# Performance work log

Measured on AMD Instinct MI355X. Metric: run time of the kernel, lower is better.

Reference implementation:

```python
import jax, jax.numpy as jnp
import numpy as np

V, E, L, H = 128, 512, 8, 8
B, T = 4, 1024
EPS = 0.1  # label smoothing


def _ln(x, s, b):
    mu = x.mean(-1, keepdims=True)
    var = ((x - mu) ** 2).mean(-1, keepdims=True)
    return (x - mu) * jax.lax.rsqrt(var + 1e-5) * s + b


def _forward(inputs, targets, emb, qkv_w, qkv_b, aff1_w, aff1_b, aff2_w, aff2_b,
             ffn1_w, ffn1_b, ffn2_w, ffn2_b, ln1_s, ln1_b, ln2_s, ln2_b, head_w, head_b):
    Bx, Tx = inputs.shape
    x = emb[inputs]                                  # [B,T,E]
    dh = E // H
    mask = jnp.tril(jnp.ones((Tx, Tx), dtype=x.dtype))
    scale = np.float32(1.0 / np.sqrt(dh))
    for l in range(L):
        qkv = x @ qkv_w[l].T + qkv_b[l]              # [B,T,3E]
        qkv = qkv.reshape(Bx, Tx, H, 3 * dh).transpose(0, 2, 1, 3)  # [B,H,T,3dh]
        q, k, v = jnp.split(qkv, 3, axis=-1)
        # NOTE: original multiplies scores by boolean tril mask (zeros, not -inf)
        scores = jnp.einsum('bhqd,bhkd->bhqk', q, k) * mask * scale
        att = jax.nn.softmax(scores, axis=-1) @ v    # [B,H,T,dh]
        att = att.transpose(0, 2, 1, 3).reshape(Bx, Tx, E)
        att = jax.nn.relu(att @ aff1_w[l].T + aff1_b[l]) @ aff2_w[l].T + aff2_b[l]
        out1 = _ln(att + x, ln1_s[l], ln1_b[l])
        out2 = jax.nn.relu(out1 @ ffn1_w[l].T + ffn1_b[l]) @ ffn2_w[l].T + ffn2_b[l]
        x = _ln(out1 + out2, ln2_s[l], ln2_b[l])
    logits = x @ head_w.T + head_b                   # [B,T,V]
    logp = jax.nn.log_softmax(logits, axis=-1)
    nll = -jnp.take_along_axis(logp, targets[..., None], axis=-1)[..., 0]
    smooth = -logp.mean(-1)
    loss = jnp.mean((1.0 - EPS) * nll + EPS * smooth)
    return logits, loss


def setup_inputs() -> dict:
    key = jax.random.key(0)
    ks = jax.random.split(key, 16)
    s = lambda k, shape, fan: (jax.random.normal(k, shape, jnp.float32) / np.sqrt(fan)).astype(jnp.float32)
    return {
        'inputs': jax.random.randint(ks[0], (B, T), 0, V, dtype=jnp.int32).astype(jnp.int64),
        'targets': jax.random.randint(ks[1], (B, T), 0, V, dtype=jnp.int32).astype(jnp.int64),
        'emb': s(ks[2], (V, E), 1.0),
        'qkv_w': s(ks[3], (L, 3 * E, E), E),
        'qkv_b': jnp.zeros((L, 3 * E), jnp.float32),
        'aff1_w': s(ks[4], (L, E, E), E),
        'aff1_b': jnp.zeros((L, E), jnp.float32),
        'aff2_w': s(ks[5], (L, E, E), E),
        'aff2_b': jnp.zeros((L, E), jnp.float32),
        'ffn1_w': s(ks[6], (L, E, E), E),
        'ffn1_b': jnp.zeros((L, E), jnp.float32),
        'ffn2_w': s(ks[7], (L, E, E), E),
        'ffn2_b': jnp.zeros((L, E), jnp.float32),
        'ln1_s': jnp.ones((L, E), jnp.float32),
        'ln1_b': jnp.zeros((L, E), jnp.float32),
        'ln2_s': jnp.ones((L, E), jnp.float32),
        'ln2_b': jnp.zeros((L, E), jnp.float32),
        'head_w': s(ks[8], (V, E), E),
        'head_b': jnp.zeros((V,), jnp.float32),
    }


def reference(inputs, targets, emb, qkv_w, qkv_b, aff1_w, aff1_b, aff2_w, aff2_b,
              ffn1_w, ffn1_b, ffn2_w, ffn2_b, ln1_s, ln1_b, ln2_s, ln2_b, head_w, head_b):
    return _forward(inputs, targets, emb, qkv_w, qkv_b, aff1_w, aff1_b, aff2_w, aff2_b,
                    ffn1_w, ffn1_b, ffn2_w, ffn2_b, ln1_s, ln1_b, ln2_s, ln2_b, head_w, head_b)
```

## Files before the change

kernel.cpp:

```cpp
#include <hip/hip_runtime.h>


#define V_  128
#define E_  512
#define L_  8
#define H_  8
#define B_  4
#define T_  1024
#define N_  (B_*T_)
#define DH_ 64
#define E3_ 1536

typedef __attribute__((ext_vector_type(8))) short   bf16x8;
typedef __attribute__((ext_vector_type(4))) float   floatx4;

#define SW(row,k8) (((row) << 6) + ((((k8) ^ ((row) & 7))) << 3))

__device__ __forceinline__ unsigned short f2bf(float f) {
    union { float f; unsigned int i; } v; v.f = f;
    unsigned int x = v.i;
    return (unsigned short)((x + 0x7fffu + ((x >> 16) & 1u)) >> 16);
}
__device__ __forceinline__ float bf2f(unsigned short u) {
    union { unsigned int i; float f; } v; v.i = ((unsigned int)u) << 16; return v.f;
}
__device__ __forceinline__ void gload_lds16(const void* g, void* l) {
    __builtin_amdgcn_global_load_lds(
        (const __attribute__((address_space(1))) unsigned int*)g,
        (__attribute__((address_space(3))) unsigned int*)l, 16, 0, 0);
}

#define CVT_N0 6291456
#define CVT_N1 2097152
#define CVT_TOT (CVT_N0 + 4*CVT_N1 + V_*E_)
__global__ void cvt_all_kernel(const float* __restrict__ s0, const float* __restrict__ s1,
                               const float* __restrict__ s2, const float* __restrict__ s3,
                               const float* __restrict__ s4, const float* __restrict__ s5,
                               unsigned short* __restrict__ dst) {
    long i = (long)(blockIdx.x * blockDim.x + threadIdx.x) * 4;
    if (i >= CVT_TOT) return;
    const float* src; long off;
    if      (i < CVT_N0)               { src = s0; off = i; }
    else if (i < CVT_N0 + CVT_N1)      { src = s1; off = i - CVT_N0; }
    else if (i < CVT_N0 + 2*CVT_N1)    { src = s2; off = i - CVT_N0 - CVT_N1; }
    else if (i < CVT_N0 + 3*CVT_N1)    { src = s3; off = i - CVT_N0 - 2L*CVT_N1; }
    else if (i < CVT_N0 + 4*CVT_N1)    { src = s4; off = i - CVT_N0 - 3L*CVT_N1; }
    else                               { src = s5; off = i - CVT_N0 - 4L*CVT_N1; }
    float4 v = *(const float4*)(src + off);
    ushort4 o; o.x = f2bf(v.x); o.y = f2bf(v.y); o.z = f2bf(v.z); o.w = f2bf(v.w);
    *(ushort4*)(dst + i) = o;
}

__global__ void embed_kernel(const int* __restrict__ tok, const float* __restrict__ emb,
                             float* __restrict__ xf, unsigned short* __restrict__ xb) {
    int idx = blockIdx.x * blockDim.x + threadIdx.x;
    if (idx >= N_ * E_) return;
    int n = idx >> 9;
    int e = idx & (E_ - 1);
    float v = emb[tok[n] * E_ + e];
    xf[idx] = v; xb[idx] = f2bf(v);
}

template<int BM, int RELU, int WF, int WB>
__global__ __launch_bounds__(256) void gemm_mfma(
    const unsigned short* __restrict__ A, const unsigned short* __restrict__ W,
    const float* __restrict__ bias, float* __restrict__ Cf, unsigned short* __restrict__ Cb,
    int M, int Nout, int K)
{
    constexpr int MI = BM / 64;
    __shared__ unsigned short Asm[2][BM * 64];
    __shared__ unsigned short Bsm[2][64 * 64];
    int tid = threadIdx.x;
    int wv = tid >> 6, ln = tid & 63;
    int lquad = ln >> 4, lmod = ln & 15;
    int m0 = blockIdx.y * BM, n0 = blockIdx.x * 64;

    floatx4 acc[MI][4] = {};

    auto stage = [&](int k0, int pb) {
        #pragma unroll
        for (int c = 0; c < BM / 32; ++c) {
            int cc = tid + 256 * c;
            int r = cc >> 3, k8s = (cc & 7) ^ (r & 7);
            gload_lds16(A + (size_t)(m0 + r) * K + k0 + 8 * k8s,
                        &Asm[pb][2048 * c + 512 * wv]);
        }
        #pragma unroll
        for (int c = 0; c < 2; ++c) {
            int cc = tid + 256 * c;
            int r = cc >> 3, k8s = (cc & 7) ^ (r & 7);
            gload_lds16(W + (size_t)(n0 + r) * K + k0 + 8 * k8s,
                        &Bsm[pb][2048 * c + 512 * wv]);
        }
    };

    int nt = K >> 6;
    stage(0, 0);
    __syncthreads();

    for (int t = 0; t < nt; ++t) {
        int pb = t & 1;
        if (t + 1 < nt) stage((t + 1) << 6, pb ^ 1);
        #pragma unroll
        for (int ks = 0; ks < 2; ++ks) {
            bf16x8 af[MI], bfr[4];
            #pragma unroll
            for (int i = 0; i < MI; ++i)
                af[i] = *(const bf16x8*)&Asm[pb][SW((BM/4) * wv + 16 * i + lmod, ks * 4 + lquad)];
            #pragma unroll
            for (int j = 0; j < 4; ++j)
                bfr[j] = *(const bf16x8*)&Bsm[pb][SW(16 * j + lmod, ks * 4 + lquad)];
            #pragma unroll
            for (int i = 0; i < MI; ++i)
                #pragma unroll
                for (int j = 0; j < 4; ++j)
                    acc[i][j] = __builtin_amdgcn_mfma_f32_16x16x32_bf16(af[i], bfr[j], acc[i][j], 0, 0, 0);
        }
        if (t + 1 < nt) __syncthreads();
    }

    #pragma unroll
    for (int i = 0; i < MI; ++i)
        #pragma unroll
        for (int j = 0; j < 4; ++j) {
            int n = n0 + 16 * j + lmod;
            float bj = bias[n];
            #pragma unroll
            for (int v = 0; v < 4; ++v) {
                int m = m0 + (BM/4) * wv + 16 * i + 4 * lquad + v;
                float val = acc[i][j][v] + bj;
                if (RELU) val = fmaxf(val, 0.f);
                if (WF) Cf[(size_t)m * Nout + n] = val;
                if (WB) Cb[(size_t)m * Nout + n] = f2bf(val);
            }
        }
}

__global__ __launch_bounds__(256) void gemm_qkv(
    const unsigned short* __restrict__ A, const unsigned short* __restrict__ W,
    const float* __restrict__ bias, unsigned short* __restrict__ Cb,
    unsigned short* __restrict__ vt_g, float* __restrict__ vtile, int K)
{
    __shared__ unsigned short Asm[2][128 * 64];
    __shared__ unsigned short Bsm[2][64 * 64];
    __shared__ float vred[4][64];
    int tid = threadIdx.x;
    int wv = tid >> 6, ln = tid & 63;
    int lquad = ln >> 4, lmod = ln & 15;
    int m0 = blockIdx.y * 128, n0 = blockIdx.x * 64;

    floatx4 acc[2][4] = {};

    auto stage = [&](int k0, int pb) {
        #pragma unroll
        for (int c = 0; c < 4; ++c) {
            int cc = tid + 256 * c;
            int r = cc >> 3, k8s = (cc & 7) ^ (r & 7);
            gload_lds16(A + (size_t)(m0 + r) * K + k0 + 8 * k8s,
                        &Asm[pb][2048 * c + 512 * wv]);
        }
        #pragma unroll
        for (int c = 0; c < 2; ++c) {
            int cc = tid + 256 * c;
            int r = cc >> 3, k8s = (cc & 7) ^ (r & 7);
            gload_lds16(W + (size_t)(n0 + r) * K + k0 + 8 * k8s,
                        &Bsm[pb][2048 * c + 512 * wv]);
        }
    };

    int nt = K >> 6;
    stage(0, 0);
    __syncthreads();
    for (int t = 0; t < nt; ++t) {
        int pb = t & 1;
        if (t + 1 < nt) stage((t + 1) << 6, pb ^ 1);
        #pragma unroll
        for (int ks = 0; ks < 2; ++ks) {
            bf16x8 af[2], bfr[4];
            #pragma unroll
            for (int i = 0; i < 2; ++i)
                af[i] = *(const bf16x8*)&Asm[pb][SW(32 * wv + 16 * i + lmod, ks * 4 + lquad)];
            #pragma unroll
            for (int j = 0; j < 4; ++j)
                bfr[j] = *(const bf16x8*)&Bsm[pb][SW(16 * j + lmod, ks * 4 + lquad)];
            #pragma unroll
            for (int i = 0; i < 2; ++i)
                #pragma unroll
                for (int j = 0; j < 4; ++j)
                    acc[i][j] = __builtin_amdgcn_mfma_f32_16x16x32_bf16(af[i], bfr[j], acc[i][j], 0, 0, 0);
        }
        if (t + 1 < nt) __syncthreads();
    }

    if ((n0 % 192) != 128) {
        #pragma unroll
        for (int i = 0; i < 2; ++i)
            #pragma unroll
            for (int j = 0; j < 4; ++j) {
                int n = n0 + 16 * j + lmod;
                float bj = bias[n];
                #pragma unroll
                for (int v = 0; v < 4; ++v) {
                    int m = m0 + 32 * wv + 16 * i + 4 * lquad + v;
                    Cb[(size_t)m * E3_ + n] = f2bf(acc[i][j][v] + bj);
                }
            }
    } else {
        int h = n0 / 192;
        int b = m0 >> 10;
        int bh = b * 8 + h;
        int t0 = m0 & 1023;
        int kt0 = t0 >> 6;
        float sj[4] = {0.f, 0.f, 0.f, 0.f};
        #pragma unroll
        for (int j = 0; j < 4; ++j) {
            float bj = bias[n0 + 16 * j + lmod];
            #pragma unroll
            for (int i = 0; i < 2; ++i) {
                union { unsigned short u[4]; uint2 q; } pk;
                #pragma unroll
                for (int v = 0; v < 4; ++v) {
                    unsigned short r = f2bf(acc[i][j][v] + bj);
                    pk.u[v] = r;
                    sj[j] += bf2f(r);
                }
                int t = t0 + 32 * wv + 16 * i + 4 * lquad;
                *(uint2*)&vt_g[((size_t)(bh * 64 + 16 * j + lmod)) * T_ + t] = pk.q;
            }
        }
        #pragma unroll
        for (int j = 0; j < 4; ++j) {
            sj[j] += __shfl_xor(sj[j], 16);
            sj[j] += __shfl_xor(sj[j], 32);
        }
        if (lquad == 0) {
            #pragma unroll
            for (int j = 0; j < 4; ++j) vred[wv][16 * j + lmod] = sj[j];
        }
        __syncthreads();
        if (tid < 128) {
            int half = tid >> 6, d = tid & 63;
            vtile[((size_t)bh * 16 + kt0 + half) * 64 + d] =
                vred[2 * half][d] + vred[2 * half + 1][d];
        }
    }
}

__global__ __launch_bounds__(256) void attn_mfma(const unsigned short* __restrict__ qkv,
                                                 const unsigned short* __restrict__ vt_g,
                                                 const float* __restrict__ vtile,
                                                 unsigned short* __restrict__ outb)
{
    __shared__ unsigned short Qs[64 * 64];
    __shared__ unsigned short Ks[2][64 * 64];
    __shared__ unsigned short Vs[2][64 * 64];
    __shared__ unsigned short Ps[64 * 64];

    int tid = threadIdx.x;
    int wv = tid >> 6, ln = tid & 63;
    int lquad = ln >> 4, lmod = ln & 15;
    int bh = blockIdx.x;
    int y = blockIdx.y;
    int qt = (y < 8) ? y : 23 - y;
    int b = bh >> 3, h = bh & 7;
    int q0 = qt * 64;
    const float scale = 0.125f;
    size_t base = (size_t)b * T_ * E3_ + h * 192;

    auto stageKV = [&](int k0, int pb) {
        #pragma unroll
        for (int c = 0; c < 2; ++c) {
            int cc = tid + 256 * c;
            int r = cc >> 3, k8s = (cc & 7) ^ (r & 7);
            gload_lds16(qkv + base + (size_t)(k0 + r) * E3_ + 64 + 8 * k8s,
                        &Ks[pb][2048 * c + 512 * wv]);
            gload_lds16(vt_g + ((size_t)(bh * 64 + r)) * T_ + k0 + 8 * k8s,
                        &Vs[pb][2048 * c + 512 * wv]);
        }
    };

    #pragma unroll
    for (int c = 0; c < 2; ++c) {
        int cc = tid + 256 * c;
        int r = cc >> 3, k8s = (cc & 7) ^ (r & 7);
        gload_lds16(qkv + base + (size_t)(q0 + r) * E3_ + 8 * k8s, Qs + 2048 * c + 512 * wv);
    }
    stageKV(0, 0);
    __syncthreads();

    float lrow[4] = {0.f, 0.f, 0.f, 0.f};
    floatx4 Oa[4] = {};

    for (int kt = 0; kt <= qt; ++kt) {
        int pb = kt & 1;
        int k0 = kt * 64;
        if (kt < qt) stageKV(k0 + 64, pb ^ 1);

        floatx4 sacc[4] = {};
        #pragma unroll
        for (int ks = 0; ks < 2; ++ks) {
            bf16x8 aq = *(const bf16x8*)&Qs[SW(16 * wv + lmod, ks * 4 + lquad)];
            #pragma unroll
            for (int j = 0; j < 4; ++j) {
                bf16x8 bk = *(const bf16x8*)&Ks[pb][SW(16 * j + lmod, ks * 4 + lquad)];
                sacc[j] = __builtin_amdgcn_mfma_f32_16x16x32_bf16(aq, bk, sacc[j], 0, 0, 0);
            }
        }
        #pragma unroll
        for (int v = 0; v < 4; ++v) {
            int qg = q0 + 16 * wv + 4 * lquad + v;
            int row = 16 * wv + 4 * lquad + v;
            #pragma unroll
            for (int j = 0; j < 4; ++j) {
                int kg = k0 + 16 * j + lmod;
                float p = (kg <= qg) ? __expf(sacc[j][v] * scale) : 1.0f;
                lrow[v] += p;
                int col = 16 * j + lmod;
                Ps[SW(row, col >> 3) + (col & 7)] = f2bf(p);
            }
        }
        asm volatile("s_waitcnt lgkmcnt(0)" ::: "memory");
        __builtin_amdgcn_s_barrier();

        #pragma unroll
        for (int ks = 0; ks < 2; ++ks) {
            bf16x8 ap = *(const bf16x8*)&Ps[SW(16 * wv + lmod, ks * 4 + lquad)];
            #pragma unroll
            for (int f = 0; f < 4; ++f) {
                bf16x8 bv = *(const bf16x8*)&Vs[pb][SW(16 * f + lmod, ks * 4 + lquad)];
                Oa[f] = __builtin_amdgcn_mfma_f32_16x16x32_bf16(ap, bv, Oa[f], 0, 0, 0);
            }
        }
        if (kt < qt) __syncthreads();
    }

    #pragma unroll
    for (int v = 0; v < 4; ++v)
        #pragma unroll
        for (int msk = 1; msk < 16; msk <<= 1) lrow[v] += __shfl_xor(lrow[v], msk);

    if (qt < 15) {
        float Km = (float)((15 - qt) * 64);
        #pragma unroll
        for (int v = 0; v < 4; ++v) lrow[v] += Km;
        #pragma unroll
        for (int f = 0; f < 4; ++f) {
            float sv = 0.f;
            for (int kt = qt + 1; kt < 16; ++kt)
                sv += vtile[((size_t)bh * 16 + kt) * 64 + 16 * f + lmod];
            #pragma unroll
            for (int v = 0; v < 4; ++v) Oa[f][v] += sv;
        }
    }

    #pragma unroll
    for (int f = 0; f < 4; ++f)
        #pragma unroll
        for (int v = 0; v < 4; ++v) {
            int q = q0 + 16 * wv + 4 * lquad + v;
            outb[(size_t)(b * T_ + q) * E_ + h * DH_ + 16 * f + lmod] = f2bf(Oa[f][v] / lrow[v]);
        }
}

__global__ __launch_bounds__(256) void add_ln_kernel(
    const float* __restrict__ a, const float* __restrict__ r,
    const float* __restrict__ s, const float* __restrict__ bpar,
    float* __restrict__ outF, unsigned short* __restrict__ outB)
{
    int tid = threadIdx.x, wv = tid >> 6, ln = tid & 63;
    int n = blockIdx.x * 4 + wv;
    int e = ln * 8;
    size_t base = (size_t)n * E_ + e;
    float4 a0 = *(const float4*)&a[base],     a1 = *(const float4*)&a[base + 4];
    float4 r0 = *(const float4*)&r[base],     r1 = *(const float4*)&r[base + 4];
    float v[8] = {a0.x + r0.x, a0.y + r0.y, a0.z + r0.z, a0.w + r0.w,
                  a1.x + r1.x, a1.y + r1.y, a1.z + r1.z, a1.w + r1.w};

    float sm = 0.f;
    #pragma unroll
    for (int i = 0; i < 8; ++i) sm += v[i];
    #pragma unroll
    for (int msk = 1; msk < 64; msk <<= 1) sm += __shfl_xor(sm, msk);
    float mu = sm * (1.f / 512.f);

    float ss = 0.f;
    #pragma unroll
    for (int i = 0; i < 8; ++i) { v[i] -= mu; ss += v[i] * v[i]; }
    #pragma unroll
    for (int msk = 1; msk < 64; msk <<= 1) ss += __shfl_xor(ss, msk);
    float rstd = rsqrtf(ss * (1.f / 512.f) + 1e-5f);

    float4 sc0 = *(const float4*)&s[e],    sc1 = *(const float4*)&s[e + 4];
    float4 bp0 = *(const float4*)&bpar[e], bp1 = *(const float4*)&bpar[e + 4];
    float o[8];
    o[0] = v[0] * rstd * sc0.x + bp0.x; o[1] = v[1] * rstd * sc0.y + bp0.y;
    o[2] = v[2] * rstd * sc0.z + bp0.z; o[3] = v[3] * rstd * sc0.w + bp0.w;
    o[4] = v[4] * rstd * sc1.x + bp1.x; o[5] = v[5] * rstd * sc1.y + bp1.y;
    o[6] = v[6] * rstd * sc1.z + bp1.z; o[7] = v[7] * rstd * sc1.w + bp1.w;
    *(float4*)&outF[base]     = make_float4(o[0], o[1], o[2], o[3]);
    *(float4*)&outF[base + 4] = make_float4(o[4], o[5], o[6], o[7]);
    union { unsigned short u[8]; uint4 q; } pk;
    #pragma unroll
    for (int i = 0; i < 8; ++i) pk.u[i] = f2bf(o[i]);
    *(uint4*)&outB[base] = pk.q;
}

__global__ __launch_bounds__(128) void loss_row_kernel(
    const float* __restrict__ logits, const int* __restrict__ tgt,
    float* __restrict__ out_logits, float* __restrict__ rowloss)
{
    int n = blockIdx.x, i = threadIdx.x;
    float x = logits[(size_t)n * V_ + i];
    out_logits[(size_t)n * V_ + i] = x;

    __shared__ float redA[2], redB[2];
    __shared__ float xt;
    int lane = i & 63, w = i >> 6;
    if (i == tgt[n]) xt = x;

    float m = x;
    #pragma unroll
    for (int off = 32; off; off >>= 1) m = fmaxf(m, __shfl_down(m, off, 64));
    if (lane == 0) redA[w] = m;
    __syncthreads();
    m = fmaxf(redA[0], redA[1]);
    __syncthreads();

    float ev = __expf(x - m);
    float se = ev, sx = x;
    #pragma unroll
    for (int off = 32; off; off >>= 1) {
        se += __shfl_down(se, off, 64);
        sx += __shfl_down(sx, off, 64);
    }
    if (lane == 0) { redA[w] = se; redB[w] = sx; }
    __syncthreads();
    if (i == 0) {
        float seT = redA[0] + redA[1], sxT = redB[0] + redB[1];
        float lse = m + __logf(seT);
        float nll = lse - xt;
        float smooth = lse - sxT * (1.f / 128.f);
        rowloss[n] = 0.9f * nll + 0.1f * smooth;
    }
}

__global__ __launch_bounds__(256) void loss_reduce_kernel(
    const float* __restrict__ rowloss, float* __restrict__ out)
{
    int tid = threadIdx.x;
    float sm = 0.f;
    for (int idx = tid; idx < N_; idx += 256) sm += rowloss[idx];
    #pragma unroll
    for (int off = 32; off; off >>= 1) sm += __shfl_down(sm, off, 64);
    __shared__ float red[4];
    int lane = tid & 63, w = tid >> 6;
    if (lane == 0) red[w] = sm;
    __syncthreads();
    if (tid == 0) out[0] = (red[0] + red[1] + red[2] + red[3]) * (1.f / (float)N_);
}

extern "C" void kernel_launch(void* const* d_in, const int* in_sizes, int n_in,
                              void* d_out, int out_size, void* d_ws, size_t ws_size,
                              hipStream_t stream)
{
    (void)in_sizes; (void)n_in; (void)out_size; (void)ws_size;
    const int* toks     = (const int*)d_in[0];
    const int* tgts     = (const int*)d_in[1];
    const float* emb    = (const float*)d_in[2];
    const float* qkv_w  = (const float*)d_in[3];
    const float* qkv_b  = (const float*)d_in[4];
    const float* aff1_w = (const float*)d_in[5];
    const float* aff1_b = (const float*)d_in[6];
    const float* aff2_w = (const float*)d_in[7];
    const float* aff2_b = (const float*)d_in[8];
    const float* ffn1_w = (const float*)d_in[9];
    const float* ffn1_b = (const float*)d_in[10];
    const float* ffn2_w = (const float*)d_in[11];
    const float* ffn2_b = (const float*)d_in[12];
    const float* ln1_s  = (const float*)d_in[13];
    const float* ln1_b  = (const float*)d_in[14];
    const float* ln2_s  = (const float*)d_in[15];
    const float* ln2_b  = (const float*)d_in[16];
    const float* head_w = (const float*)d_in[17];
    const float* head_b = (const float*)d_in[18];

    char* p = (char*)d_ws;
    auto carve = [&](size_t bytes) { char* r = p; p += (bytes + 255) & ~(size_t)255; return (void*)r; };
    unsigned short* wb_all  = (unsigned short*)carve((size_t)CVT_TOT * 2);
    unsigned short* wb_qkv  = wb_all;
    unsigned short* wb_aff1 = wb_qkv  + (size_t)CVT_N0;
    unsigned short* wb_aff2 = wb_aff1 + (size_t)CVT_N1;
    unsigned short* wb_ffn1 = wb_aff2 + (size_t)CVT_N1;
    unsigned short* wb_ffn2 = wb_ffn1 + (size_t)CVT_N1;
    unsigned short* wb_head = wb_ffn2 + (size_t)CVT_N1;
    float*          x_f     = (float*)carve((size_t)N_ * E_ * 4);
    unsigned short* x_b     = (unsigned short*)carve((size_t)N_ * E_ * 2);
    unsigned short* qkv_bf  = (unsigned short*)carve((size_t)N_ * E3_ * 2);
    unsigned short* att_b   = (unsigned short*)carve((size_t)N_ * E_ * 2);
    unsigned short* h_b     = (unsigned short*)carve((size_t)N_ * E_ * 2);
    float*          y_f     = (float*)carve((size_t)N_ * E_ * 4);
    float*          o1_f    = (float*)carve((size_t)N_ * E_ * 4);
    unsigned short* o1_b    = (unsigned short*)carve((size_t)N_ * E_ * 2);
    float*          logits  = (float*)carve((size_t)N_ * V_ * 4);
    float*          rowl    = (float*)carve((size_t)N_ * 4);
    float*          vtile   = (float*)carve((size_t)32 * 16 * 64 * 4);
    unsigned short* vt_g    = (unsigned short*)carve((size_t)32 * 64 * T_ * 2);

    float* out_logits = (float*)d_out;
    float* out_loss   = out_logits + (size_t)N_ * V_;

    cvt_all_kernel<<<dim3(CVT_TOT / 1024), 256, 0, stream>>>(
        qkv_w, aff1_w, aff2_w, ffn1_w, ffn2_w, head_w, wb_all);

    embed_kernel<<<dim3((N_ * E_) / 256), 256, 0, stream>>>(toks, emb, x_f, x_b);

    for (int l = 0; l < L_; ++l) {
        gemm_qkv<<<dim3(E3_/64, N_/128), 256, 0, stream>>>(
            x_b, wb_qkv + (size_t)l * E3_ * E_, qkv_b + (size_t)l * E3_,
            qkv_bf, vt_g, vtile, E_);
        attn_mfma<<<dim3(32, 16), 256, 0, stream>>>(qkv_bf, vt_g, vtile, att_b);
        gemm_mfma<64,1,0,1><<<dim3(E_/64, N_/64), 256, 0, stream>>>(
            att_b, wb_aff1 + (size_t)l * E_ * E_, aff1_b + (size_t)l * E_,
            nullptr, h_b, N_, E_, E_);
        gemm_mfma<64,0,1,0><<<dim3(E_/64, N_/64), 256, 0, stream>>>(
            h_b, wb_aff2 + (size_t)l * E_ * E_, aff2_b + (size_t)l * E_,
            y_f, nullptr, N_, E_, E_);
        add_ln_kernel<<<dim3(N_/4), 256, 0, stream>>>(
            y_f, x_f, ln1_s + (size_t)l * E_, ln1_b + (size_t)l * E_, o1_f, o1_b);
        gemm_mfma<64,1,0,1><<<dim3(E_/64, N_/64), 256, 0, stream>>>(
            o1_b, wb_ffn1 + (size_t)l * E_ * E_, ffn1_b + (size_t)l * E_,
            nullptr, h_b, N_, E_, E_);
        gemm_mfma<64,0,1,0><<<dim3(E_/64, N_/64), 256, 0, stream>>>(
            h_b, wb_ffn2 + (size_t)l * E_ * E_, ffn2_b + (size_t)l * E_,
            y_f, nullptr, N_, E_, E_);
        add_ln_kernel<<<dim3(N_/4), 256, 0, stream>>>(
            o1_f, y_f, ln2_s + (size_t)l * E_, ln2_b + (size_t)l * E_, x_f, x_b);
    }

    gemm_mfma<64,0,1,0><<<dim3(V_/64, N_/64), 256, 0, stream>>>(
        x_b, wb_head, head_b, logits, nullptr, N_, V_, E_);
    loss_row_kernel<<<dim3(N_), 128, 0, stream>>>(logits, tgts, out_logits, rowl);
    loss_reduce_kernel<<<dim3(1), 256, 0, stream>>>(rowl, out_loss);
}
```

Measured before the change: 843.3 us.

## Fuse two-layer MLP with residual LayerNorm, and head GEMM with loss

```diff
diff --git a/kernel.cpp b/kernel.cpp
--- a/kernel.cpp
+++ b/kernel.cpp
@@ -61,81 +61,6 @@
     xf[idx] = v; xb[idx] = f2bf(v);
 }
 
-template<int BM, int RELU, int WF, int WB>
-__global__ __launch_bounds__(256) void gemm_mfma(
-    const unsigned short* __restrict__ A, const unsigned short* __restrict__ W,
-    const float* __restrict__ bias, float* __restrict__ Cf, unsigned short* __restrict__ Cb,
-    int M, int Nout, int K)
-{
-    constexpr int MI = BM / 64;
-    __shared__ unsigned short Asm[2][BM * 64];
-    __shared__ unsigned short Bsm[2][64 * 64];
-    int tid = threadIdx.x;
-    int wv = tid >> 6, ln = tid & 63;
-    int lquad = ln >> 4, lmod = ln & 15;
-    int m0 = blockIdx.y * BM, n0 = blockIdx.x * 64;
-
-    floatx4 acc[MI][4] = {};
-
-    auto stage = [&](int k0, int pb) {
-        #pragma unroll
-        for (int c = 0; c < BM / 32; ++c) {
-            int cc = tid + 256 * c;
-            int r = cc >> 3, k8s = (cc & 7) ^ (r & 7);
-            gload_lds16(A + (size_t)(m0 + r) * K + k0 + 8 * k8s,
-                        &Asm[pb][2048 * c + 512 * wv]);
-        }
-        #pragma unroll
-        for (int c = 0; c < 2; ++c) {
-            int cc = tid + 256 * c;
-            int r = cc >> 3, k8s = (cc & 7) ^ (r & 7);
-            gload_lds16(W + (size_t)(n0 + r) * K + k0 + 8 * k8s,
-                        &Bsm[pb][2048 * c + 512 * wv]);
-        }
-    };
-
-    int nt = K >> 6;
-    stage(0, 0);
-    __syncthreads();
-
-    for (int t = 0; t < nt; ++t) {
-        int pb = t & 1;
-        if (t + 1 < nt) stage((t + 1) << 6, pb ^ 1);
-        #pragma unroll
-        for (int ks = 0; ks < 2; ++ks) {
-            bf16x8 af[MI], bfr[4];
-            #pragma unroll
-            for (int i = 0; i < MI; ++i)
-                af[i] = *(const bf16x8*)&Asm[pb][SW((BM/4) * wv + 16 * i + lmod, ks * 4 + lquad)];
-            #pragma unroll
-            for (int j = 0; j < 4; ++j)
-                bfr[j] = *(const bf16x8*)&Bsm[pb][SW(16 * j + lmod, ks * 4 + lquad)];
-            #pragma unroll
-            for (int i = 0; i < MI; ++i)
-                #pragma unroll
-                for (int j = 0; j < 4; ++j)
-                    acc[i][j] = __builtin_amdgcn_mfma_f32_16x16x32_bf16(af[i], bfr[j], acc[i][j], 0, 0, 0);
-        }
-        if (t + 1 < nt) __syncthreads();
-    }
-
-    #pragma unroll
-    for (int i = 0; i < MI; ++i)
-        #pragma unroll
-        for (int j = 0; j < 4; ++j) {
-            int n = n0 + 16 * j + lmod;
-            float bj = bias[n];
-            #pragma unroll
-            for (int v = 0; v < 4; ++v) {
-                int m = m0 + (BM/4) * wv + 16 * i + 4 * lquad + v;
-                float val = acc[i][j][v] + bj;
-                if (RELU) val = fmaxf(val, 0.f);
-                if (WF) Cf[(size_t)m * Nout + n] = val;
-                if (WB) Cb[(size_t)m * Nout + n] = f2bf(val);
-            }
-        }
-}
-
 __global__ __launch_bounds__(256) void gemm_qkv(
     const unsigned short* __restrict__ A, const unsigned short* __restrict__ W,
     const float* __restrict__ bias, unsigned short* __restrict__ Cb,
@@ -362,85 +287,197 @@
         }
 }
 
-__global__ __launch_bounds__(256) void add_ln_kernel(
-    const float* __restrict__ a, const float* __restrict__ r,
-    const float* __restrict__ s, const float* __restrict__ bpar,
+__global__ __launch_bounds__(1024) void fused_mlp_ln(
+    const unsigned short* __restrict__ A, const float* __restrict__ resF,
+    const unsigned short* __restrict__ W1, const float* __restrict__ b1,
+    const unsigned short* __restrict__ W2, const float* __restrict__ b2,
+    const float* __restrict__ lns, const float* __restrict__ lnb,
     float* __restrict__ outF, unsigned short* __restrict__ outB)
 {
-    int tid = threadIdx.x, wv = tid >> 6, ln = tid & 63;
-    int n = blockIdx.x * 4 + wv;
-    int e = ln * 8;
-    size_t base = (size_t)n * E_ + e;
-    float4 a0 = *(const float4*)&a[base],     a1 = *(const float4*)&a[base + 4];
-    float4 r0 = *(const float4*)&r[base],     r1 = *(const float4*)&r[base + 4];
-    float v[8] = {a0.x + r0.x, a0.y + r0.y, a0.z + r0.z, a0.w + r0.w,
-                  a1.x + r1.x, a1.y + r1.y, a1.z + r1.z, a1.w + r1.w};
-
-    float sm = 0.f;
-    #pragma unroll
-    for (int i = 0; i < 8; ++i) sm += v[i];
-    #pragma unroll
-    for (int msk = 1; msk < 64; msk <<= 1) sm += __shfl_xor(sm, msk);
-    float mu = sm * (1.f / 512.f);
-
-    float ss = 0.f;
-    #pragma unroll
-    for (int i = 0; i < 8; ++i) { v[i] -= mu; ss += v[i] * v[i]; }
-    #pragma unroll
-    for (int msk = 1; msk < 64; msk <<= 1) ss += __shfl_xor(ss, msk);
-    float rstd = rsqrtf(ss * (1.f / 512.f) + 1e-5f);
-
-    float4 sc0 = *(const float4*)&s[e],    sc1 = *(const float4*)&s[e + 4];
-    float4 bp0 = *(const float4*)&bpar[e], bp1 = *(const float4*)&bpar[e + 4];
-    float o[8];
-    o[0] = v[0] * rstd * sc0.x + bp0.x; o[1] = v[1] * rstd * sc0.y + bp0.y;
-    o[2] = v[2] * rstd * sc0.z + bp0.z; o[3] = v[3] * rstd * sc0.w + bp0.w;
-    o[4] = v[4] * rstd * sc1.x + bp1.x; o[5] = v[5] * rstd * sc1.y + bp1.y;
-    o[6] = v[6] * rstd * sc1.z + bp1.z; o[7] = v[7] * rstd * sc1.w + bp1.w;
-    *(float4*)&outF[base]     = make_float4(o[0], o[1], o[2], o[3]);
-    *(float4*)&outF[base + 4] = make_float4(o[4], o[5], o[6], o[7]);
-    union { unsigned short u[8]; uint4 q; } pk;
-    #pragma unroll
-    for (int i = 0; i < 8; ++i) pk.u[i] = f2bf(o[i]);
-    *(uint4*)&outB[base] = pk.q;
-}
-
-__global__ __launch_bounds__(128) void loss_row_kernel(
-    const float* __restrict__ logits, const int* __restrict__ tgt,
+    __shared__ unsigned short Asl[16 * 512];
+    __shared__ unsigned short Hsl[16 * 512];
+    __shared__ float red[16][16];
+    __shared__ float stat[2][16];
+
+    int tid = threadIdx.x;
+    int wv = tid >> 6, ln = tid & 63;
+    int lquad = ln >> 4, lmod = ln & 15;
+    int m0 = blockIdx.x * 16;
+
+    gload_lds16(A + (size_t)(m0 + wv) * E_ + ((ln ^ (wv & 7)) << 3),
+                Asl + (wv << 9));
+    __syncthreads();
+
+    int c0 = (wv << 5) + lmod, c1 = c0 + 16;
+
+    floatx4 a0 = {0.f, 0.f, 0.f, 0.f}, a1 = {0.f, 0.f, 0.f, 0.f};
+    #pragma unroll
+    for (int ki = 0; ki < 16; ++ki) {
+        int k8 = (ki << 2) + lquad;
+        bf16x8 af = *(const bf16x8*)&Asl[(lmod << 9) + ((k8 ^ (lmod & 7)) << 3)];
+        bf16x8 w0 = *(const bf16x8*)&W1[(size_t)c0 * E_ + (k8 << 3)];
+        bf16x8 w1 = *(const bf16x8*)&W1[(size_t)c1 * E_ + (k8 << 3)];
+        a0 = __builtin_amdgcn_mfma_f32_16x16x32_bf16(af, w0, a0, 0, 0, 0);
+        a1 = __builtin_amdgcn_mfma_f32_16x16x32_bf16(af, w1, a1, 0, 0, 0);
+    }
+    float bb0 = b1[c0], bb1 = b1[c1];
+    #pragma unroll
+    for (int v = 0; v < 4; ++v) {
+        int row = (lquad << 2) + v;
+        Hsl[(row << 9) + (((c0 >> 3) ^ (row & 7)) << 3) + (lmod & 7)] =
+            f2bf(fmaxf(a0[v] + bb0, 0.f));
+        Hsl[(row << 9) + (((c1 >> 3) ^ (row & 7)) << 3) + (lmod & 7)] =
+            f2bf(fmaxf(a1[v] + bb1, 0.f));
+    }
+    __syncthreads();
+
+    floatx4 y0 = {0.f, 0.f, 0.f, 0.f}, y1 = {0.f, 0.f, 0.f, 0.f};
+    #pragma unroll
+    for (int ki = 0; ki < 16; ++ki) {
+        int k8 = (ki << 2) + lquad;
+        bf16x8 hf = *(const bf16x8*)&Hsl[(lmod << 9) + ((k8 ^ (lmod & 7)) << 3)];
+        bf16x8 w0 = *(const bf16x8*)&W2[(size_t)c0 * E_ + (k8 << 3)];
+        bf16x8 w1 = *(const bf16x8*)&W2[(size_t)c1 * E_ + (k8 << 3)];
+        y0 = __builtin_amdgcn_mfma_f32_16x16x32_bf16(hf, w0, y0, 0, 0, 0);
+        y1 = __builtin_amdgcn_mfma_f32_16x16x32_bf16(hf, w1, y1, 0, 0, 0);
+    }
+    float b20 = b2[c0], b21 = b2[c1];
+    float z0[4], z1[4];
+    #pragma unroll
+    for (int v = 0; v < 4; ++v) {
+        int gm = m0 + (lquad << 2) + v;
+        z0[v] = y0[v] + b20 + resF[(size_t)gm * E_ + c0];
+        z1[v] = y1[v] + b21 + resF[(size_t)gm * E_ + c1];
+    }
+    #pragma unroll
+    for (int v = 0; v < 4; ++v) {
+        float s = z0[v] + z1[v];
+        s += __shfl_xor(s, 1); s += __shfl_xor(s, 2);
+        s += __shfl_xor(s, 4); s += __shfl_xor(s, 8);
+        if (lmod == 0) red[(lquad << 2) + v][wv] = s;
+    }
+    __syncthreads();
+    if (tid < 16) {
+        float s = 0.f;
+        #pragma unroll
+        for (int w = 0; w < 16; ++w) s += red[tid][w];
+        stat[0][tid] = s * (1.f / 512.f);
+    }
+    __syncthreads();
+    #pragma unroll
+    for (int v = 0; v < 4; ++v) {
+        int row = (lquad << 2) + v;
+        float mu = stat[0][row];
+        float d0 = z0[v] - mu, d1 = z1[v] - mu;
+        float s = d0 * d0 + d1 * d1;
+        s += __shfl_xor(s, 1); s += __shfl_xor(s, 2);
+        s += __shfl_xor(s, 4); s += __shfl_xor(s, 8);
+        if (lmod == 0) red[row][wv] = s;
+    }
+    __syncthreads();
+    if (tid < 16) {
+        float s = 0.f;
+        #pragma unroll
+        for (int w = 0; w < 16; ++w) s += red[tid][w];
+        stat[1][tid] = rsqrtf(s * (1.f / 512.f) + 1e-5f);
+    }
+    __syncthreads();
+    float s0 = lns[c0], s1 = lns[c1], p0 = lnb[c0], p1 = lnb[c1];
+    #pragma unroll
+    for (int v = 0; v < 4; ++v) {
+        int row = (lquad << 2) + v;
+        int gm = m0 + row;
+        float mu = stat[0][row], rs = stat[1][row];
+        float o0 = (z0[v] - mu) * rs * s0 + p0;
+        float o1 = (z1[v] - mu) * rs * s1 + p1;
+        outF[(size_t)gm * E_ + c0] = o0;
+        outF[(size_t)gm * E_ + c1] = o1;
+        outB[(size_t)gm * E_ + c0] = f2bf(o0);
+        outB[(size_t)gm * E_ + c1] = f2bf(o1);
+    }
+}
+
+__global__ __launch_bounds__(256) void head_loss_kernel(
+    const unsigned short* __restrict__ A, const unsigned short* __restrict__ W,
+    const float* __restrict__ bias, const int* __restrict__ tgt,
     float* __restrict__ out_logits, float* __restrict__ rowloss)
 {
-    int n = blockIdx.x, i = threadIdx.x;
-    float x = logits[(size_t)n * V_ + i];
-    out_logits[(size_t)n * V_ + i] = x;
-
-    __shared__ float redA[2], redB[2];
-    __shared__ float xt;
-    int lane = i & 63, w = i >> 6;
-    if (i == tgt[n]) xt = x;
-
-    float m = x;
-    #pragma unroll
-    for (int off = 32; off; off >>= 1) m = fmaxf(m, __shfl_down(m, off, 64));
-    if (lane == 0) redA[w] = m;
-    __syncthreads();
-    m = fmaxf(redA[0], redA[1]);
-    __syncthreads();
-
-    float ev = __expf(x - m);
-    float se = ev, sx = x;
-    #pragma unroll
-    for (int off = 32; off; off >>= 1) {
-        se += __shfl_down(se, off, 64);
-        sx += __shfl_down(sx, off, 64);
-    }
-    if (lane == 0) { redA[w] = se; redB[w] = sx; }
-    __syncthreads();
-    if (i == 0) {
-        float seT = redA[0] + redA[1], sxT = redB[0] + redB[1];
-        float lse = m + __logf(seT);
-        float nll = lse - xt;
-        float smooth = lse - sxT * (1.f / 128.f);
-        rowloss[n] = 0.9f * nll + 0.1f * smooth;
+    __shared__ unsigned short Asm[2][64 * 64];
+    __shared__ unsigned short Bsm[2][128 * 64];
+    int tid = threadIdx.x;
+    int wv = tid >> 6, ln = tid & 63;
+    int lquad = ln >> 4, lmod = ln & 15;
+    int m0 = blockIdx.x * 64;
+
+    floatx4 acc[8] = {};
+
+    auto stage = [&](int k0, int pb) {
+        #pragma unroll
+        for (int c = 0; c < 2; ++c) {
+            int cc = tid + 256 * c;
+            int r = cc >> 3, k8s = (cc & 7) ^ (r & 7);
+            gload_lds16(A + (size_t)(m0 + r) * E_ + k0 + 8 * k8s,
+                        &Asm[pb][2048 * c + 512 * wv]);
+        }
+        #pragma unroll
+        for (int c = 0; c < 4; ++c) {
+            int cc = tid + 256 * c;
+            int r = cc >> 3, k8s = (cc & 7) ^ (r & 7);
+            gload_lds16(W + (size_t)r * E_ + k0 + 8 * k8s,
+                        &Bsm[pb][2048 * c + 512 * wv]);
+        }
+    };
+
+    stage(0, 0);
+    __syncthreads();
+    for (int t = 0; t < 8; ++t) {
+        int pb = t & 1;
+        if (t < 7) stage((t + 1) << 6, pb ^ 1);
+        #pragma unroll
+        for (int ks = 0; ks < 2; ++ks) {
+            bf16x8 af = *(const bf16x8*)&Asm[pb][SW(16 * wv + lmod, ks * 4 + lquad)];
+            #pragma unroll
+            for (int j = 0; j < 8; ++j) {
+                bf16x8 bf = *(const bf16x8*)&Bsm[pb][SW(16 * j + lmod, ks * 4 + lquad)];
+                acc[j] = __builtin_amdgcn_mfma_f32_16x16x32_bf16(af, bf, acc[j], 0, 0, 0);
+            }
+        }
+        if (t < 7) __syncthreads();
+    }
+
+    float bj[8];
+    #pragma unroll
+    for (int j = 0; j < 8; ++j) bj[j] = bias[16 * j + lmod];
+    #pragma unroll
+    for (int v = 0; v < 4; ++v) {
+        int m = m0 + 16 * wv + 4 * lquad + v;
+        float x[8];
+        float mx = -1e30f, sx = 0.f;
+        #pragma unroll
+        for (int j = 0; j < 8; ++j) {
+            x[j] = acc[j][v] + bj[j];
+            out_logits[(size_t)m * V_ + 16 * j + lmod] = x[j];
+            mx = fmaxf(mx, x[j]); sx += x[j];
+        }
+        #pragma unroll
+        for (int msk = 1; msk < 16; msk <<= 1) mx = fmaxf(mx, __shfl_xor(mx, msk));
+        float se = 0.f;
+        #pragma unroll
+        for (int j = 0; j < 8; ++j) se += __expf(x[j] - mx);
+        #pragma unroll
+        for (int msk = 1; msk < 16; msk <<= 1) {
+            se += __shfl_xor(se, msk);
+            sx += __shfl_xor(sx, msk);
+        }
+        int t = tgt[m];
+        float cand = 0.f;
+        #pragma unroll
+        for (int j = 0; j < 8; ++j) cand = ((t >> 4) == j) ? x[j] : cand;
+        float xt = __shfl(cand, (ln & 48) | (t & 15));
+        if (lmod == 0) {
+            float lse = mx + __logf(se);
+            rowloss[m] = 0.9f * (lse - xt) + 0.1f * (lse - sx * (1.f / 128.f));
+        }
     }
 }
 
@@ -497,11 +534,8 @@
     unsigned short* x_b     = (unsigned short*)carve((size_t)N_ * E_ * 2);
     unsigned short* qkv_bf  = (unsigned short*)carve((size_t)N_ * E3_ * 2);
     unsigned short* att_b   = (unsigned short*)carve((size_t)N_ * E_ * 2);
-    unsigned short* h_b     = (unsigned short*)carve((size_t)N_ * E_ * 2);
-    float*          y_f     = (float*)carve((size_t)N_ * E_ * 4);
     float*          o1_f    = (float*)carve((size_t)N_ * E_ * 4);
     unsigned short* o1_b    = (unsigned short*)carve((size_t)N_ * E_ * 2);
-    float*          logits  = (float*)carve((size_t)N_ * V_ * 4);
     float*          rowl    = (float*)carve((size_t)N_ * 4);
     float*          vtile   = (float*)carve((size_t)32 * 16 * 64 * 4);
     unsigned short* vt_g    = (unsigned short*)carve((size_t)32 * 64 * T_ * 2);
@@ -519,26 +553,21 @@
             x_b, wb_qkv + (size_t)l * E3_ * E_, qkv_b + (size_t)l * E3_,
             qkv_bf, vt_g, vtile, E_);
         attn_mfma<<<dim3(32, 16), 256, 0, stream>>>(qkv_bf, vt_g, vtile, att_b);
-        gemm_mfma<64,1,0,1><<<dim3(E_/64, N_/64), 256, 0, stream>>>(
-            att_b, wb_aff1 + (size_t)l * E_ * E_, aff1_b + (size_t)l * E_,
-            nullptr, h_b, N_, E_, E_);
-        gemm_mfma<64,0,1,0><<<dim3(E_/64, N_/64), 256, 0, stream>>>(
-            h_b, wb_aff2 + (size_t)l * E_ * E_, aff2_b + (size_t)l * E_,
-            y_f, nullptr, N_, E_, E_);
-        add_ln_kernel<<<dim3(N_/4), 256, 0, stream>>>(
-            y_f, x_f, ln1_s + (size_t)l * E_, ln1_b + (size_t)l * E_, o1_f, o1_b);
-        gemm_mfma<64,1,0,1><<<dim3(E_/64, N_/64), 256, 0, stream>>>(
-            o1_b, wb_ffn1 + (size_t)l * E_ * E_, ffn1_b + (size_t)l * E_,
-            nullptr, h_b, N_, E_, E_);
-        gemm_mfma<64,0,1,0><<<dim3(E_/64, N_/64), 256, 0, stream>>>(
-            h_b, wb_ffn2 + (size_t)l * E_ * E_, ffn2_b + (size_t)l * E_,
-            y_f, nullptr, N_, E_, E_);
-        add_ln_kernel<<<dim3(N_/4), 256, 0, stream>>>(
-            o1_f, y_f, ln2_s + (size_t)l * E_, ln2_b + (size_t)l * E_, x_f, x_b);
-    }
-
-    gemm_mfma<64,0,1,0><<<dim3(V_/64, N_/64), 256, 0, stream>>>(
-        x_b, wb_head, head_b, logits, nullptr, N_, V_, E_);
-    loss_row_kernel<<<dim3(N_), 128, 0, stream>>>(logits, tgts, out_logits, rowl);
+        fused_mlp_ln<<<dim3(N_/16), 1024, 0, stream>>>(
+            att_b, x_f,
+            wb_aff1 + (size_t)l * E_ * E_, aff1_b + (size_t)l * E_,
+            wb_aff2 + (size_t)l * E_ * E_, aff2_b + (size_t)l * E_,
+            ln1_s + (size_t)l * E_, ln1_b + (size_t)l * E_,
+            o1_f, o1_b);
+        fused_mlp_ln<<<dim3(N_/16), 1024, 0, stream>>>(
+            o1_b, o1_f,
+            wb_ffn1 + (size_t)l * E_ * E_, ffn1_b + (size_t)l * E_,
+            wb_ffn2 + (size_t)l * E_ * E_, ffn2_b + (size_t)l * E_,
+            ln2_s + (size_t)l * E_, ln2_b + (size_t)l * E_,
+            x_f, x_b);
+    }
+
+    head_loss_kernel<<<dim3(N_/64), 256, 0, stream>>>(
+        x_b, wb_head, head_b, tgts, out_logits, rowl);
     loss_reduce_kernel<<<dim3(1), 256, 0, stream>>>(rowl, out_loss);
 }
```

New measurement: 1.003 ms. 1.19x slower.

## Fuse head GEMM with loss, deepen GEMM K pipeline to 128 per barrier

Applied to the files above, without the earlier changes.

```diff
diff --git a/kernel.cpp b/kernel.cpp
--- a/kernel.cpp
+++ b/kernel.cpp
@@ -61,79 +61,77 @@
     xf[idx] = v; xb[idx] = f2bf(v);
 }
 
-template<int BM, int RELU, int WF, int WB>
-__global__ __launch_bounds__(256) void gemm_mfma(
+template<int RELU, int WF, int WB>
+__global__ __launch_bounds__(256) void gemm64(
     const unsigned short* __restrict__ A, const unsigned short* __restrict__ W,
     const float* __restrict__ bias, float* __restrict__ Cf, unsigned short* __restrict__ Cb,
     int M, int Nout, int K)
 {
-    constexpr int MI = BM / 64;
-    __shared__ unsigned short Asm[2][BM * 64];
-    __shared__ unsigned short Bsm[2][64 * 64];
+    __shared__ unsigned short Asm[4][64 * 64];
+    __shared__ unsigned short Bsm[4][64 * 64];
     int tid = threadIdx.x;
     int wv = tid >> 6, ln = tid & 63;
     int lquad = ln >> 4, lmod = ln & 15;
-    int m0 = blockIdx.y * BM, n0 = blockIdx.x * 64;
-
-    floatx4 acc[MI][4] = {};
-
-    auto stage = [&](int k0, int pb) {
-        #pragma unroll
-        for (int c = 0; c < BM / 32; ++c) {
+    int m0 = blockIdx.y * 64, n0 = blockIdx.x * 64;
+
+    floatx4 acc[4] = {};
+
+    auto stage = [&](int k0, int s) {
+        #pragma unroll
+        for (int c = 0; c < 2; ++c) {
             int cc = tid + 256 * c;
             int r = cc >> 3, k8s = (cc & 7) ^ (r & 7);
             gload_lds16(A + (size_t)(m0 + r) * K + k0 + 8 * k8s,
-                        &Asm[pb][2048 * c + 512 * wv]);
+                        &Asm[s][2048 * c + 512 * wv]);
         }
         #pragma unroll
         for (int c = 0; c < 2; ++c) {
             int cc = tid + 256 * c;
             int r = cc >> 3, k8s = (cc & 7) ^ (r & 7);
             gload_lds16(W + (size_t)(n0 + r) * K + k0 + 8 * k8s,
-                        &Bsm[pb][2048 * c + 512 * wv]);
+                        &Bsm[s][2048 * c + 512 * wv]);
         }
     };
 
-    int nt = K >> 6;
+    int np = K >> 7;
     stage(0, 0);
+    stage(64, 1);
     __syncthreads();
 
-    for (int t = 0; t < nt; ++t) {
-        int pb = t & 1;
-        if (t + 1 < nt) stage((t + 1) << 6, pb ^ 1);
-        #pragma unroll
-        for (int ks = 0; ks < 2; ++ks) {
-            bf16x8 af[MI], bfr[4];
-            #pragma unroll
-            for (int i = 0; i < MI; ++i)
-                af[i] = *(const bf16x8*)&Asm[pb][SW((BM/4) * wv + 16 * i + lmod, ks * 4 + lquad)];
-            #pragma unroll
-            for (int j = 0; j < 4; ++j)
-                bfr[j] = *(const bf16x8*)&Bsm[pb][SW(16 * j + lmod, ks * 4 + lquad)];
-            #pragma unroll
-            for (int i = 0; i < MI; ++i)
+    for (int t = 0; t < np; ++t) {
+        if (t + 1 < np) {
+            stage((2 * t + 2) << 6, (2 * t + 2) & 3);
+            stage((2 * t + 3) << 6, (2 * t + 3) & 3);
+        }
+        #pragma unroll
+        for (int half = 0; half < 2; ++half) {
+            int s = (2 * t + half) & 3;
+            #pragma unroll
+            for (int ks = 0; ks < 2; ++ks) {
+                bf16x8 af = *(const bf16x8*)&Asm[s][SW(16 * wv + lmod, ks * 4 + lquad)];
                 #pragma unroll
-                for (int j = 0; j < 4; ++j)
-                    acc[i][j] = __builtin_amdgcn_mfma_f32_16x16x32_bf16(af[i], bfr[j], acc[i][j], 0, 0, 0);
-        }
-        if (t + 1 < nt) __syncthreads();
-    }
-
-    #pragma unroll
-    for (int i = 0; i < MI; ++i)
-        #pragma unroll
-        for (int j = 0; j < 4; ++j) {
-            int n = n0 + 16 * j + lmod;
-            float bj = bias[n];
-            #pragma unroll
-            for (int v = 0; v < 4; ++v) {
-                int m = m0 + (BM/4) * wv + 16 * i + 4 * lquad + v;
-                float val = acc[i][j][v] + bj;
-                if (RELU) val = fmaxf(val, 0.f);
-                if (WF) Cf[(size_t)m * Nout + n] = val;
-                if (WB) Cb[(size_t)m * Nout + n] = f2bf(val);
-            }
-        }
+                for (int j = 0; j < 4; ++j) {
+                    bf16x8 bfr = *(const bf16x8*)&Bsm[s][SW(16 * j + lmod, ks * 4 + lquad)];
+                    acc[j] = __builtin_amdgcn_mfma_f32_16x16x32_bf16(af, bfr, acc[j], 0, 0, 0);
+                }
+            }
+        }
+        if (t + 1 < np) __syncthreads();
+    }
+
+    #pragma unroll
+    for (int j = 0; j < 4; ++j) {
+        int n = n0 + 16 * j + lmod;
+        float bj = bias[n];
+        #pragma unroll
+        for (int v = 0; v < 4; ++v) {
+            int m = m0 + 16 * wv + 4 * lquad + v;
+            float val = acc[j][v] + bj;
+            if (RELU) val = fmaxf(val, 0.f);
+            if (WF) Cf[(size_t)m * Nout + n] = val;
+            if (WB) Cb[(size_t)m * Nout + n] = f2bf(val);
+        }
+    }
 }
 
 __global__ __launch_bounds__(256) void gemm_qkv(
@@ -405,42 +403,87 @@
     *(uint4*)&outB[base] = pk.q;
 }
 
-__global__ __launch_bounds__(128) void loss_row_kernel(
-    const float* __restrict__ logits, const int* __restrict__ tgt,
+__global__ __launch_bounds__(256) void head_loss_kernel(
+    const unsigned short* __restrict__ A, const unsigned short* __restrict__ W,
+    const float* __restrict__ bias, const int* __restrict__ tgt,
     float* __restrict__ out_logits, float* __restrict__ rowloss)
 {
-    int n = blockIdx.x, i = threadIdx.x;
-    float x = logits[(size_t)n * V_ + i];
-    out_logits[(size_t)n * V_ + i] = x;
-
-    __shared__ float redA[2], redB[2];
-    __shared__ float xt;
-    int lane = i & 63, w = i >> 6;
-    if (i == tgt[n]) xt = x;
-
-    float m = x;
-    #pragma unroll
-    for (int off = 32; off; off >>= 1) m = fmaxf(m, __shfl_down(m, off, 64));
-    if (lane == 0) redA[w] = m;
+    __shared__ unsigned short Asm[2][64 * 64];
+    __shared__ unsigned short Bsm[2][128 * 64];
+    int tid = threadIdx.x;
+    int wv = tid >> 6, ln = tid & 63;
+    int lquad = ln >> 4, lmod = ln & 15;
+    int m0 = blockIdx.x * 64;
+
+    floatx4 acc[8] = {};
+
+    auto stage = [&](int k0, int pb) {
+        #pragma unroll
+        for (int c = 0; c < 2; ++c) {
+            int cc = tid + 256 * c;
+            int r = cc >> 3, k8s = (cc & 7) ^ (r & 7);
+            gload_lds16(A + (size_t)(m0 + r) * E_ + k0 + 8 * k8s,
+                        &Asm[pb][2048 * c + 512 * wv]);
+        }
+        #pragma unroll
+        for (int c = 0; c < 4; ++c) {
+            int cc = tid + 256 * c;
+            int r = cc >> 3, k8s = (cc & 7) ^ (r & 7);
+            gload_lds16(W + (size_t)r * E_ + k0 + 8 * k8s,
+                        &Bsm[pb][2048 * c + 512 * wv]);
+        }
+    };
+
+    stage(0, 0);
     __syncthreads();
-    m = fmaxf(redA[0], redA[1]);
-    __syncthreads();
-
-    float ev = __expf(x - m);
-    float se = ev, sx = x;
-    #pragma unroll
-    for (int off = 32; off; off >>= 1) {
-        se += __shfl_down(se, off, 64);
-        sx += __shfl_down(sx, off, 64);
-    }
-    if (lane == 0) { redA[w] = se; redB[w] = sx; }
-    __syncthreads();
-    if (i == 0) {
-        float seT = redA[0] + redA[1], sxT = redB[0] + redB[1];
-        float lse = m + __logf(seT);
-        float nll = lse - xt;
-        float smooth = lse - sxT * (1.f / 128.f);
-        rowloss[n] = 0.9f * nll + 0.1f * smooth;
+    for (int t = 0; t < 8; ++t) {
+        int pb = t & 1;
+        if (t < 7) stage((t + 1) << 6, pb ^ 1);
+        #pragma unroll
+        for (int ks = 0; ks < 2; ++ks) {
+            bf16x8 af = *(const bf16x8*)&Asm[pb][SW(16 * wv + lmod, ks * 4 + lquad)];
+            #pragma unroll
+            for (int j = 0; j < 8; ++j) {
+                bf16x8 bf = *(const bf16x8*)&Bsm[pb][SW(16 * j + lmod, ks * 4 + lquad)];
+                acc[j] = __builtin_amdgcn_mfma_f32_16x16x32_bf16(af, bf, acc[j], 0, 0, 0);
+            }
+        }
+        if (t < 7) __syncthreads();
+    }
+
+    float bj[8];
+    #pragma unroll
+    for (int j = 0; j < 8; ++j) bj[j] = bias[16 * j + lmod];
+    #pragma unroll
+    for (int v = 0; v < 4; ++v) {
+        int m = m0 + 16 * wv + 4 * lquad + v;
+        float x[8];
+        float mx = -1e30f, sx = 0.f;
+        #pragma unroll
+        for (int j = 0; j < 8; ++j) {
+            x[j] = acc[j][v] + bj[j];
+            out_logits[(size_t)m * V_ + 16 * j + lmod] = x[j];
+            mx = fmaxf(mx, x[j]); sx += x[j];
+        }
+        #pragma unroll
+        for (int msk = 1; msk < 16; msk <<= 1) mx = fmaxf(mx, __shfl_xor(mx, msk));
+        float se = 0.f;
+        #pragma unroll
+        for (int j = 0; j < 8; ++j) se += __expf(x[j] - mx);
+        #pragma unroll
+        for (int msk = 1; msk < 16; msk <<= 1) {
+            se += __shfl_xor(se, msk);
+            sx += __shfl_xor(sx, msk);
+        }
+        int t = tgt[m];
+        float cand = 0.f;
+        #pragma unroll
+        for (int j = 0; j < 8; ++j) cand = ((t >> 4) == j) ? x[j] : cand;
+        float xt = __shfl(cand, (ln & 48) | (t & 15));
+        if (lmod == 0) {
+            float lse = mx + __logf(se);
+            rowloss[m] = 0.9f * (lse - xt) + 0.1f * (lse - sx * (1.f / 128.f));
+        }
     }
 }
 
@@ -501,7 +544,6 @@
     float*          y_f     = (float*)carve((size_t)N_ * E_ * 4);
     float*          o1_f    = (float*)carve((size_t)N_ * E_ * 4);
     unsigned short* o1_b    = (unsigned short*)carve((size_t)N_ * E_ * 2);
-    float*          logits  = (float*)carve((size_t)N_ * V_ * 4);
     float*          rowl    = (float*)carve((size_t)N_ * 4);
     float*          vtile   = (float*)carve((size_t)32 * 16 * 64 * 4);
     unsigned short* vt_g    = (unsigned short*)carve((size_t)32 * 64 * T_ * 2);
@@ -519,26 +561,25 @@
             x_b, wb_qkv + (size_t)l * E3_ * E_, qkv_b + (size_t)l * E3_,
             qkv_bf, vt_g, vtile, E_);
         attn_mfma<<<dim3(32, 16), 256, 0, stream>>>(qkv_bf, vt_g, vtile, att_b);
-        gemm_mfma<64,1,0,1><<<dim3(E_/64, N_/64), 256, 0, stream>>>(
+        gemm64<1,0,1><<<dim3(E_/64, N_/64), 256, 0, stream>>>(
             att_b, wb_aff1 + (size_t)l * E_ * E_, aff1_b + (size_t)l * E_,
             nullptr, h_b, N_, E_, E_);
-        gemm_mfma<64,0,1,0><<<dim3(E_/64, N_/64), 256, 0, stream>>>(
+        gemm64<0,1,0><<<dim3(E_/64, N_/64), 256, 0, stream>>>(
             h_b, wb_aff2 + (size_t)l * E_ * E_, aff2_b + (size_t)l * E_,
             y_f, nullptr, N_, E_, E_);
         add_ln_kernel<<<dim3(N_/4), 256, 0, stream>>>(
             y_f, x_f, ln1_s + (size_t)l * E_, ln1_b + (size_t)l * E_, o1_f, o1_b);
-        gemm_mfma<64,1,0,1><<<dim3(E_/64, N_/64), 256, 0, stream>>>(
+        gemm64<1,0,1><<<dim3(E_/64, N_/64), 256, 0, stream>>>(
             o1_b, wb_ffn1 + (size_t)l * E_ * E_, ffn1_b + (size_t)l * E_,
             nullptr, h_b, N_, E_, E_);
-        gemm_mfma<64,0,1,0><<<dim3(E_/64, N_/64), 256, 0, stream>>>(
+        gemm64<0,1,0><<<dim3(E_/64, N_/64), 256, 0, stream>>>(
             h_b, wb_ffn2 + (size_t)l * E_ * E_, ffn2_b + (size_t)l * E_,
             y_f, nullptr, N_, E_, E_);
         add_ln_kernel<<<dim3(N_/4), 256, 0, stream>>>(
             o1_f, y_f, ln2_s + (size_t)l * E_, ln2_b + (size_t)l * E_, x_f, x_b);
     }
 
-    gemm_mfma<64,0,1,0><<<dim3(V_/64, N_/64), 256, 0, stream>>>(
-        x_b, wb_head, head_b, logits, nullptr, N_, V_, E_);
-    loss_row_kernel<<<dim3(N_), 128, 0, stream>>>(logits, tgts, out_logits, rowl);
+    head_loss_kernel<<<dim3(N_/64), 256, 0, stream>>>(
+        x_b, wb_head, head_b, tgts, out_logits, rowl);
     loss_reduce_kernel<<<dim3(1), 256, 0, stream>>>(rowl, out_loss);
 }
```

After: 815.5 us. 1.03x faster.
